# Performance work log

Hardware: AMD Instinct MI355X
Metric: run time of the kernel (lower is better)

Reference implementation:

```python
import jax, jax.numpy as jnp
import numpy as np

CONF_THRES = 0.25
IOU_THRES = 0.45
MAX_DET = 100      # yolov5 max_det passed in forward()
K_PRE = 1024       # pre-NMS candidate cap (yolov5 uses 30000; capped for O(k^2) IoU)
MAX_WH = 7680.0    # yolov5 class-offset trick for non-agnostic NMS
EPS = 1e-7


def _xywh2xyxy(b):
    # b: [k, 4] (cx, cy, w, h) -> (x1, y1, x2, y2)
    cx, cy, w, h = b[:, 0], b[:, 1], b[:, 2], b[:, 3]
    return jnp.stack([cx - w * 0.5, cy - h * 0.5, cx + w * 0.5, cy + h * 0.5], axis=-1)


def _iou_matrix(boxes):
    # boxes: [k, 4] xyxy -> [k, k] pairwise IoU
    lt = jnp.maximum(boxes[:, None, :2], boxes[None, :, :2])
    rb = jnp.minimum(boxes[:, None, 2:], boxes[None, :, 2:])
    wh = jnp.clip(rb - lt, 0.0)
    inter = wh[..., 0] * wh[..., 1]
    area = (boxes[:, 2] - boxes[:, 0]) * (boxes[:, 3] - boxes[:, 1])
    union = area[:, None] + area[None, :] - inter
    return inter / (union + EPS)


def _nms_single(pred):
    # pred: [N, 5+nc] = (cx, cy, w, h, obj, cls...)
    obj = pred[:, 4]
    cls_conf = pred[:, 5:] * obj[:, None]          # obj * cls, yolov5 conf
    score = jnp.max(cls_conf, axis=-1)             # best-class score
    cls = jnp.argmax(cls_conf, axis=-1)
    valid = (obj > CONF_THRES) & (score > CONF_THRES)

    # top K_PRE candidates by score (invalid -> -1)
    s_masked = jnp.where(valid, score, -1.0)
    scores_t, idx = jax.lax.top_k(s_masked, K_PRE)  # sorted descending
    boxes = _xywh2xyxy(pred[idx, :4])               # [K_PRE, 4]
    cls_t = cls[idx].astype(pred.dtype)
    valid_t = scores_t > 0.0

    # class offset so different classes never overlap (agnostic=False)
    iou = _iou_matrix(boxes + cls_t[:, None] * MAX_WH)

    # greedy sequential suppression over score-sorted candidates
    idxr = jnp.arange(K_PRE)

    def step(keep, xs):
        i, iou_row = xs
        sup = jnp.any((iou_row > IOU_THRES) & keep & (idxr < i))
        keep = keep.at[i].set(keep[i] & ~sup)
        return keep, None

    keep, _ = jax.lax.scan(step, valid_t, (idxr, iou))

    # gather up to MAX_DET kept detections (already score-sorted)
    sk = jnp.where(keep, scores_t, -1.0)
    sel_scores, sel = jax.lax.top_k(sk, MAX_DET)
    det = jnp.concatenate(
        [boxes[sel], scores_t[sel][:, None], cls_t[sel][:, None]], axis=-1)  # [MAX_DET, 6]
    det = jnp.where((sel_scores > 0.0)[:, None], det, 0.0)
    return det


def setup_inputs() -> dict:
    key = jax.random.key(0)
    B, N, C = 8, 100800, 85  # img_size=1280, 3 anchors, strides 8/16/32; nc=80
    pred = jax.random.uniform(key, (B, N, C), dtype=jnp.float32)
    # put box coords in pixel range [0, 640); scores stay in [0, 1)
    pred = pred.at[..., :4].multiply(640.0)
    return {"pred": pred}


def reference(pred) -> jnp.ndarray:
    # [B, MAX_DET, 6] = (x1, y1, x2, y2, conf, cls), zero-padded
    return jax.vmap(_nms_single)(pred)
```

## Files before the change

### kernel.cpp

```cpp
#include <hip/hip_runtime.h>
#include <hip/hip_bf16.h>

typedef unsigned int u32;
typedef unsigned long long u64;

#define B 8
#define NANCH 100800
#define NCH 85
#define KPRE 1024
#define MAXDET 100
#define CONF 0.25f
#define IOU_T 0.45f
#define EPS_F 1e-7f
#define MAX_WH 7680.0f
#define CAP 4096
#define NBIN 257
#define BASEBITS 0x3E800000u

__global__ __launch_bounds__(256) void score_kernel(const float* __restrict__ pred,
                                                    u32* __restrict__ keys,
                                                    unsigned char* __restrict__ cls8,
                                                    u32* __restrict__ ghist) {
    __shared__ u32 lh[B * NBIN];
    for (int i = threadIdx.x; i < B * NBIN; i += 256) lh[i] = 0;
    __syncthreads();

    const int total = B * NANCH;
    int gtid = blockIdx.x * blockDim.x + threadIdx.x;
    int wid = gtid >> 6;
    int lane = threadIdx.x & 63;
    int nwaves = (gridDim.x * blockDim.x) >> 6;

    for (int a = wid; a < total; a += nwaves) {
        const float* p = pred + (size_t)a * NCH;
        float c1 = p[4 + lane];
        float c2 = (lane < 17) ? p[68 + lane] : 0.0f;
        float obj = __shfl(c1, 0);
        float v1 = (lane >= 1) ? c1 * obj : -1.0f;
        float v2 = (lane < 17) ? c2 * obj : -1.0f;
        float v = fmaxf(v1, v2);
        #pragma unroll
        for (int m = 1; m < 64; m <<= 1) v = fmaxf(v, __shfl_xor(v, m));
        u64 m1 = __ballot(v1 == v);
        u64 m2 = __ballot(v2 == v);
        if (lane == 0) {
            int c = m1 ? (__builtin_ctzll(m1) - 1) : (63 + __builtin_ctzll(m2));
            bool valid = (obj > CONF) && (v > CONF);
            u32 k = valid ? __float_as_uint(v) : 0u;
            keys[a] = k;
            cls8[a] = (unsigned char)c;
            if (k) {
                int b = a / NANCH;
                u32 bin = (k - BASEBITS) >> 16;
                if (bin > 256) bin = 256;
                atomicAdd(&lh[b * NBIN + bin], 1u);
            }
        }
    }
    __syncthreads();
    for (int i = threadIdx.x; i < B * NBIN; i += 256) {
        u32 v = lh[i];
        if (v) atomicAdd(&ghist[i], v);
    }
}

__global__ __launch_bounds__(1024) void select_kernel(const float* __restrict__ pred,
                                                      const u32* __restrict__ keys,
                                                      const unsigned char* __restrict__ cls8,
                                                      const u32* __restrict__ ghist,
                                                      float* __restrict__ out) {
    #pragma clang fp contract(off)
    const int b = blockIdx.x;
    const int tid = threadIdx.x;

    __shared__ u64 items[CAP];
    __shared__ float s_score[KPRE];
    __shared__ float s_cls[KPRE];
    __shared__ float4 s_box[KPRE];
    __shared__ float4 s_obox[KPRE];
    __shared__ float s_area[KPRE];
    __shared__ u32 s_hist[NBIN];
    __shared__ int s_piv;
    __shared__ int s_cnt;
    __shared__ int s_keep[MAXDET];
    __shared__ int s_nk;

    if (tid < NBIN) s_hist[tid] = ghist[b * NBIN + tid];
    if (tid == 0) s_cnt = 0;
    __syncthreads();
    if (tid == 0) {
        int cum = 0, piv = 0;
        for (int t = 256; t >= 0; --t) {
            cum += (int)s_hist[t];
            if (cum >= KPRE) { piv = t; break; }
        }
        s_piv = piv;
    }
    __syncthreads();
    const int piv = s_piv;

    const uint4* kb4 = (const uint4*)(keys + (size_t)b * NANCH);
    const int NV = NANCH / 4;
    for (int j = tid; j < NV; j += 1024) {
        uint4 kv = kb4[j];
        u32 ks[4] = {kv.x, kv.y, kv.z, kv.w};
        #pragma unroll
        for (int e = 0; e < 4; ++e) {
            u32 k = ks[e];
            if (k) {
                u32 bin = (k - BASEBITS) >> 16;
                if (bin > 256) bin = 256;
                if ((int)bin >= piv) {
                    int p = atomicAdd(&s_cnt, 1);
                    if (p < CAP) items[p] = (((u64)(~k)) << 32) | (u32)(j * 4 + e);
                }
            }
        }
    }
    __syncthreads();
    int n = s_cnt; if (n > CAP) n = CAP;

    int m = KPRE;
    while (m < n) m <<= 1;
    for (int i = tid; i < m; i += 1024)
        if (i >= n) items[i] = ~0ull;
    __syncthreads();

    for (int k = 2; k <= m; k <<= 1) {
        for (int j = k >> 1; j >= 1; j >>= 1) {
            for (int p = tid; p < m / 2; p += 1024) {
                int i = ((p & ~(j - 1)) << 1) | (p & (j - 1));
                int pr = i | j;
                bool up = ((i & k) == 0);
                u64 a = items[i], c = items[pr];
                if ((a > c) == up) { items[i] = c; items[pr] = a; }
            }
            __syncthreads();
        }
    }

    if (tid < KPRE) {
        u64 it = items[tid];
        u32 invk = (u32)(it >> 32);
        if (invk != 0xFFFFFFFFu && tid < n) {
            u32 k = ~invk;
            u32 idx = (u32)it;
            float score = __uint_as_float(k);
            const float* pb = pred + ((size_t)b * NANCH + idx) * NCH;
            float cx = pb[0], cy = pb[1], w = pb[2], h = pb[3];
            float x1 = cx - w * 0.5f;
            float y1 = cy - h * 0.5f;
            float x2 = cx + w * 0.5f;
            float y2 = cy + h * 0.5f;
            float clsf = (float)cls8[(size_t)b * NANCH + idx];
            float off = clsf * MAX_WH;
            float bx1 = x1 + off, by1 = y1 + off, bx2 = x2 + off, by2 = y2 + off;
            s_score[tid] = score;
            s_cls[tid] = clsf;
            s_box[tid] = make_float4(x1, y1, x2, y2);
            s_obox[tid] = make_float4(bx1, by1, bx2, by2);
            s_area[tid] = (bx2 - bx1) * (by2 - by1);
        } else {
            s_score[tid] = -1.0f;
            s_cls[tid] = 0.0f;
            s_box[tid] = make_float4(0.f, 0.f, 0.f, 0.f);
            s_obox[tid] = make_float4(0.f, 0.f, 0.f, 0.f);
            s_area[tid] = 0.0f;
        }
    }
    __syncthreads();

    if (tid < 64) {
        const int lane = tid;
        float4 kb0 = make_float4(0, 0, 0, 0), kb1 = kb0;
        float ka0 = 0.0f, ka1 = 0.0f;
        int kept = 0;

        float sc_n = s_score[0];
        float4 cb_n = s_obox[0];
        float ca_n = s_area[0];

        for (int i = 0; i < KPRE; ++i) {
            float sc = sc_n;
            float4 cb = cb_n;
            float ca = ca_n;
            if (i + 1 < KPRE) {
                sc_n = s_score[i + 1];
                cb_n = s_obox[i + 1];
                ca_n = s_area[i + 1];
            }
            if (sc <= 0.0f) break;

            bool sup0 = false, sup1 = false;
            if (lane < kept) {
                float ltx = fmaxf(cb.x, kb0.x);
                float lty = fmaxf(cb.y, kb0.y);
                float rbx = fminf(cb.z, kb0.z);
                float rby = fminf(cb.w, kb0.w);
                float iw = fmaxf(rbx - ltx, 0.0f);
                float ih = fmaxf(rby - lty, 0.0f);
                float inter = iw * ih;
                float uni = ca + ka0 - inter;
                sup0 = (inter / (uni + EPS_F)) > IOU_T;
            }
            if (lane + 64 < kept) {
                float ltx = fmaxf(cb.x, kb1.x);
                float lty = fmaxf(cb.y, kb1.y);
                float rbx = fminf(cb.z, kb1.z);
                float rby = fminf(cb.w, kb1.w);
                float iw = fmaxf(rbx - ltx, 0.0f);
                float ih = fmaxf(rby - lty, 0.0f);
                float inter = iw * ih;
                float uni = ca + ka1 - inter;
                sup1 = (inter / (uni + EPS_F)) > IOU_T;
            }
            u64 bal = __ballot(sup0 || sup1);
            if (bal == 0) {
                if (lane == 0) s_keep[kept] = i;
                if (kept < 64) {
                    if (lane == kept) { kb0 = cb; ka0 = ca; }
                } else {
                    if (lane == kept - 64) { kb1 = cb; ka1 = ca; }
                }
                ++kept;
                if (kept >= MAXDET) break;
            }
        }
        if (lane == 0) s_nk = kept;
    }
    __syncthreads();
    const int nk = s_nk;

    if (tid < MAXDET) {
        float o0 = 0, o1 = 0, o2 = 0, o3 = 0, o4 = 0, o5 = 0;
        if (tid < nk) {
            int i = s_keep[tid];
            float4 bx = s_box[i];
            o0 = bx.x; o1 = bx.y; o2 = bx.z; o3 = bx.w;
            o4 = s_score[i];
            o5 = s_cls[i];
        }
        float* po = out + ((size_t)b * MAXDET + tid) * 6;
        po[0] = o0; po[1] = o1; po[2] = o2; po[3] = o3; po[4] = o4; po[5] = o5;
    }
}

extern "C" void kernel_launch(void* const* d_in, const int* in_sizes, int n_in,
                              void* d_out, int out_size, void* d_ws, size_t ws_size,
                              hipStream_t stream) {
    const float* pred = (const float*)d_in[0];
    float* out = (float*)d_out;
    char* ws = (char*)d_ws;

    u32* keys           = (u32*)(ws + 0);
    unsigned char* cls8 = (unsigned char*)(ws + 3225600);
    u32* ghist          = (u32*)(ws + 4032000);

    hipMemsetAsync(ghist, 0, B * NBIN * sizeof(u32), stream);
    score_kernel<<<2048, 256, 0, stream>>>(pred, keys, cls8, ghist);
    select_kernel<<<B, 1024, 0, stream>>>(pred, keys, cls8, ghist, out);
}
```

Measured before the change: 476.8 us.

## Stage 64-row chunks through LDS so each lane scores one anchor

The score kernel now has each wave load a contiguous 64-anchor chunk with coalesced float4 loads, write it to LDS, and let each lane scan its own row of 80 classes serially. Before, a whole wave worked on one anchor with shuffle reductions and ballots, and only lane 0 wrote results. The aim is fully coalesced wide global reads and no cross-lane reduction per anchor. In exchange each wave uses about 21.8KB of LDS with strided per-lane row reads that may bank-conflict, and the grid shrinks from 2048 to 256 blocks.

```diff
diff --git a/kernel.cpp b/kernel.cpp
--- a/kernel.cpp
+++ b/kernel.cpp
@@ -17,44 +17,61 @@
 #define NBIN 257
 #define BASEBITS 0x3E800000u
 
+#define ROWS 64
+#define RDW 85
+#define CHDW (ROWS * RDW)
+#define NCHUNK (B * NANCH / ROWS)
+#define CPB (NANCH / ROWS)
+
 __global__ __launch_bounds__(256) void score_kernel(const float* __restrict__ pred,
                                                     u32* __restrict__ keys,
                                                     unsigned char* __restrict__ cls8,
                                                     u32* __restrict__ ghist) {
+    __shared__ __align__(16) float sbuf[4 * CHDW];
     __shared__ u32 lh[B * NBIN];
     for (int i = threadIdx.x; i < B * NBIN; i += 256) lh[i] = 0;
     __syncthreads();
 
-    const int total = B * NANCH;
-    int gtid = blockIdx.x * blockDim.x + threadIdx.x;
-    int wid = gtid >> 6;
-    int lane = threadIdx.x & 63;
-    int nwaves = (gridDim.x * blockDim.x) >> 6;
-
-    for (int a = wid; a < total; a += nwaves) {
-        const float* p = pred + (size_t)a * NCH;
-        float c1 = p[4 + lane];
-        float c2 = (lane < 17) ? p[68 + lane] : 0.0f;
-        float obj = __shfl(c1, 0);
-        float v1 = (lane >= 1) ? c1 * obj : -1.0f;
-        float v2 = (lane < 17) ? c2 * obj : -1.0f;
-        float v = fmaxf(v1, v2);
-        #pragma unroll
-        for (int m = 1; m < 64; m <<= 1) v = fmaxf(v, __shfl_xor(v, m));
-        u64 m1 = __ballot(v1 == v);
-        u64 m2 = __ballot(v2 == v);
-        if (lane == 0) {
-            int c = m1 ? (__builtin_ctzll(m1) - 1) : (63 + __builtin_ctzll(m2));
-            bool valid = (obj > CONF) && (v > CONF);
-            u32 k = valid ? __float_as_uint(v) : 0u;
-            keys[a] = k;
-            cls8[a] = (unsigned char)c;
-            if (k) {
-                int b = a / NANCH;
-                u32 bin = (k - BASEBITS) >> 16;
-                if (bin > 256) bin = 256;
-                atomicAdd(&lh[b * NBIN + bin], 1u);
-            }
+    const int lane = threadIdx.x & 63;
+    const int wloc = threadIdx.x >> 6;
+    float* sw = &sbuf[wloc * CHDW];
+    const int gwave = (blockIdx.x << 2) | wloc;
+    const int nwaves = gridDim.x << 2;
+
+    for (int ch = gwave; ch < NCHUNK; ch += nwaves) {
+        const float* src = pred + (size_t)ch * CHDW;
+
+        float4 r[21];
+        #pragma unroll
+        for (int i = 0; i < 21; ++i)
+            r[i] = ((const float4*)src)[i * 64 + lane];
+        float rt = src[21 * 256 + lane];
+        #pragma unroll
+        for (int i = 0; i < 21; ++i)
+            *(float4*)&sw[i * 256 + (lane << 2)] = r[i];
+        sw[21 * 256 + lane] = rt;
+
+        const float* row = &sw[lane * RDW];
+        float obj = row[4];
+        float best = -1.0f;
+        int bidx = 0;
+        #pragma unroll
+        for (int c = 0; c < 80; ++c) {
+            float v = row[5 + c] * obj;
+            bool g = v > best;
+            best = g ? v : best;
+            bidx = g ? c : bidx;
+        }
+        bool valid = (obj > CONF) & (best > CONF);
+        u32 k = valid ? __float_as_uint(best) : 0u;
+        int a = ch * ROWS + lane;
+        keys[a] = k;
+        cls8[a] = (unsigned char)bidx;
+        if (k) {
+            int b = ch / CPB;
+            u32 bin = (k - BASEBITS) >> 16;
+            if (bin > 256) bin = 256;
+            atomicAdd(&lh[b * NBIN + bin], 1u);
         }
     }
     __syncthreads();
@@ -257,6 +274,6 @@
     u32* ghist          = (u32*)(ws + 4032000);
 
     hipMemsetAsync(ghist, 0, B * NBIN * sizeof(u32), stream);
-    score_kernel<<<2048, 256, 0, stream>>>(pred, keys, cls8, ghist);
+    score_kernel<<<256, 256, 0, stream>>>(pred, keys, cls8, ghist);
     select_kernel<<<B, 1024, 0, stream>>>(pred, keys, cls8, ghist, out);
 }
```

Result: slower. 535.5 us (+12.3%).
